# Optimization experiments

Hardware: AMD Instinct MI355X
Metric: run time of the kernel (lower is better)

The kernel has to match this reference:

```python
import jax, jax.numpy as jnp
import numpy as np

E = 1_000_000   # number of multicut edges
T = 2_000_000   # number of triplets (GNN nodes)
M = 4_000_000   # number of directed GNN edges among triplets
HID = 32


def gcn_conv(x, edge_index, W, b, n):
    """PyG GCNConv: x' = D^-1/2 (A+I) D^-1/2 (x W) + b, symmetric norm with self-loops."""
    src, dst = edge_index[0], edge_index[1]
    xw = x @ W                                        # [n, out]
    deg = jnp.zeros((n,), xw.dtype).at[dst].add(1.0) + 1.0  # +1 self-loop
    dis = jax.lax.rsqrt(deg)                          # deg^-1/2
    norm = dis[src] * dis[dst]                        # [M]
    msg = xw[src] * norm[:, None]                     # gather + scale
    out = jax.ops.segment_sum(msg, dst, num_segments=n)
    out = out + xw * (dis * dis)[:, None]             # self-loop contribution
    return out + b


def setup_inputs() -> dict:
    key = jax.random.key(0)
    ks = jax.random.split(key, 16)
    inp = {
        "edge_costs": jax.random.normal(ks[0], (E,), jnp.float32),
        "t12": jax.random.normal(ks[1], (T,), jnp.float32),
        "t13": jax.random.normal(ks[2], (T,), jnp.float32),
        "t23": jax.random.normal(ks[3], (T,), jnp.float32),
        "corr_12": jax.random.randint(ks[4], (T,), 0, E),
        "corr_13": jax.random.randint(ks[5], (T,), 0, E),
        "corr_23": jax.random.randint(ks[6], (T,), 0, E),
        # counts >= 1 so the divide is well-defined (as in real triplet decompositions)
        "edge_counter": jax.random.randint(ks[7], (E,), 1, 6).astype(jnp.float32),
        "edge_index": jax.random.randint(ks[8], (2, M), 0, T),
        # GCNConv / Linear parameters (glorot-ish scale)
        "W1": jax.random.normal(ks[9], (3, HID), jnp.float32) * (1.0 / np.sqrt(3)),
        "b1": jnp.zeros((HID,), jnp.float32),
        "W2": jax.random.normal(ks[10], (HID, HID), jnp.float32) * (1.0 / np.sqrt(HID)),
        "b2": jnp.zeros((HID,), jnp.float32),
        "Wout": jax.random.normal(ks[11], (HID, 3), jnp.float32) * (1.0 / np.sqrt(HID)),
        "bout": jnp.zeros((3,), jnp.float32),
    }
    return inp


def reference(edge_costs, t12, t13, t23, corr_12, corr_13, corr_23,
              edge_counter, edge_index, W1, b1, W2, b2, Wout, bout):
    # --- send_messages_to_triplets: gather / divide, then zero covered edges ---
    t12 = t12 + edge_costs[corr_12] / edge_counter[corr_12]
    t13 = t13 + edge_costs[corr_13] / edge_counter[corr_13]
    t23 = t23 + edge_costs[corr_23] / edge_counter[corr_23]
    edge_costs = jnp.where(edge_counter > 0, jnp.zeros_like(edge_costs), edge_costs)

    # --- send_messages_to_edges: 2-layer GCN over triplet nodes + linear head ---
    tri = jnp.stack([t12, t13, t23], axis=1)          # [T, 3]
    x = jax.nn.relu(gcn_conv(tri, edge_index, W1, b1, T))
    x = jax.nn.relu(gcn_conv(x, edge_index, W2, b2, T))
    delta = x @ Wout + bout                           # [T, 3]

    t12 = t12 - delta[:, 0]
    t13 = t13 - delta[:, 1]
    t23 = t23 - delta[:, 2]

    edge_updates = (jnp.zeros_like(edge_costs)
                    .at[corr_12].add(delta[:, 0])
                    .at[corr_13].add(delta[:, 1])
                    .at[corr_23].add(delta[:, 2]))
    edge_costs = edge_costs + edge_updates
    return (edge_costs, t12, t13, t23)
```

## Files before the change

### kernel.cpp

```cpp
#include <hip/hip_runtime.h>
#include <hip/hip_fp16.h>
#include <math.h>

#define HID 32
#define BS 256

#define NPB 4096
#define NBK_MAX 1024
#define EBT 8192
#define CAP 11776

#define NPB_E 2048

typedef _Float16 h2v __attribute__((ext_vector_type(2)));

__device__ __forceinline__ h2v u2h(uint u) { return __builtin_bit_cast(h2v, u); }
__device__ __forceinline__ uint h2u(h2v h) { return __builtin_bit_cast(uint, h); }
__device__ __forceinline__ uint pack2(float a, float b) {
  h2v r; r.x = (_Float16)a; r.y = (_Float16)b; return h2u(r);
}
__device__ __forceinline__ float dot2acc(uint a, uint b, float c) {
#if __has_builtin(__builtin_amdgcn_fdot2)
  return __builtin_amdgcn_fdot2(u2h(a), u2h(b), c, false);
#else
  h2v ah = u2h(a), bh = u2h(b);
  c = fmaf((float)ah.x, (float)bh.x, c);
  return fmaf((float)ah.y, (float)bh.y, c);
#endif
}
__device__ __forceinline__ float h4w(uint2 g) {
  h2v hi = u2h(g.y); return (float)hi.y;
}


__global__ __launch_bounds__(BS) void k_bhist2(const int* __restrict__ ei,
                                               int* __restrict__ thist, int M, int NBK) {
  __shared__ int hist[NBK_MAX];
  for (int b = threadIdx.x; b < NBK; b += BS) hist[b] = 0;
  __syncthreads();
  int e0 = blockIdx.x * EBT;
  int n = min(EBT, M - e0);
  for (int k = threadIdx.x; k < n; k += BS) {
    int d = ei[M + e0 + k];
    atomicAdd(&hist[d / NPB], 1);
  }
  __syncthreads();
  for (int b = threadIdx.x; b < NBK; b += BS)
    thist[blockIdx.x * NBK + b] = hist[b];
}

__global__ __launch_bounds__(BS) void k_ehist2(const int* __restrict__ c12,
                                               const int* __restrict__ c13,
                                               const int* __restrict__ c23,
                                               int* __restrict__ thist, int T, int NBK) {
  __shared__ int hist[NBK_MAX];
  for (int b = threadIdx.x; b < NBK; b += BS) hist[b] = 0;
  __syncthreads();
  int N3 = 3 * T;
  int j0 = blockIdx.x * EBT;
  int n = min(EBT, N3 - j0);
  for (int k = threadIdx.x; k < n; k += BS) {
    int j = j0 + k;
    int key = (j < T) ? c12[j] : ((j < 2 * T) ? c13[j - T] : c23[j - 2 * T]);
    atomicAdd(&hist[key / NPB_E], 1);
  }
  __syncthreads();
  for (int b = threadIdx.x; b < NBK; b += BS)
    thist[blockIdx.x * NBK + b] = hist[b];
}

__global__ __launch_bounds__(BS) void k_tbase(const int* __restrict__ thist,
                                              int* __restrict__ tbase,
                                              int* __restrict__ gh, int NBK, int NT) {
  __shared__ int part[BS];
  int b = blockIdx.x;
  int C = (NT + BS - 1) / BS;
  int s = 0;
  for (int k = 0; k < C; ++k) {
    int t = threadIdx.x * C + k;
    if (t < NT) s += thist[t * NBK + b];
  }
  part[threadIdx.x] = s;
  __syncthreads();
  for (int off = 1; off < BS; off <<= 1) {
    int v = part[threadIdx.x];
    int u = (threadIdx.x >= off) ? part[threadIdx.x - off] : 0;
    __syncthreads();
    part[threadIdx.x] = v + u;
    __syncthreads();
  }
  int run = (threadIdx.x > 0) ? part[threadIdx.x - 1] : 0;
  for (int k = 0; k < C; ++k) {
    int t = threadIdx.x * C + k;
    if (t < NT) {
      int v = thist[t * NBK + b];
      tbase[t * NBK + b] = run;
      run += v;
    }
  }
  if (threadIdx.x == BS - 1) gh[b] = run;
}

__global__ __launch_bounds__(BS) void k_bscan(const int* __restrict__ gh,
                                              int* __restrict__ gboff,
                                              int* __restrict__ gcur, int NBK) {
  __shared__ int part[BS];
  int C = (NBK + BS - 1) / BS;
  int s = 0;
  for (int k = 0; k < C; ++k) {
    int idx = threadIdx.x * C + k;
    if (idx < NBK) s += gh[idx];
  }
  part[threadIdx.x] = s;
  __syncthreads();
  for (int off = 1; off < BS; off <<= 1) {
    int v = part[threadIdx.x];
    int u = (threadIdx.x >= off) ? part[threadIdx.x - off] : 0;
    __syncthreads();
    part[threadIdx.x] = v + u;
    __syncthreads();
  }
  int run = (threadIdx.x > 0) ? part[threadIdx.x - 1] : 0;
  for (int k = 0; k < C; ++k) {
    int idx = threadIdx.x * C + k;
    if (idx < NBK) {
      gboff[idx] = run;
      gcur[idx] = run;
      run += gh[idx];
    }
  }
  if (threadIdx.x == BS - 1) gboff[NBK] = run;
}

__global__ __launch_bounds__(BS) void k_bplace(const int* __restrict__ ei,
                                               const int* __restrict__ gboff,
                                               const int* __restrict__ tbase,
                                               int2* __restrict__ P, int M, int NBK) {
  __shared__ int cur[NBK_MAX];
  int t = blockIdx.x;
  for (int b = threadIdx.x; b < NBK; b += BS)
    cur[b] = gboff[b] + tbase[t * NBK + b];
  __syncthreads();
  int e0 = t * EBT;
  int n = min(EBT, M - e0);
  for (int k = threadIdx.x; k < n; k += BS) {
    int sidx = ei[e0 + k];
    int d = ei[M + e0 + k];
    int pos = atomicAdd(&cur[d / NPB], 1);
    P[pos] = make_int2(sidx, d);
  }
}

__global__ __launch_bounds__(BS) void k_escatv(const int* __restrict__ c12,
                                               const int* __restrict__ c13,
                                               const int* __restrict__ c23,
                                               const float* __restrict__ dd,
                                               const int* __restrict__ gboff,
                                               const int* __restrict__ tbase,
                                               int2* __restrict__ PEV, int T, int NBK) {
  __shared__ int cur[NBK_MAX];
  int t = blockIdx.x;
  for (int b = threadIdx.x; b < NBK; b += BS)
    cur[b] = gboff[b] + tbase[t * NBK + b];
  __syncthreads();
  int N3 = 3 * T;
  int j0 = t * EBT;
  int n = min(EBT, N3 - j0);
  for (int k = threadIdx.x; k < n; k += BS) {
    int j = j0 + k;
    int key = (j < T) ? c12[j] : ((j < 2 * T) ? c13[j - T] : c23[j - 2 * T]);
    float v = dd[j];
    int pos = atomicAdd(&cur[key / NPB_E], 1);
    PEV[pos] = make_int2(key, __builtin_bit_cast(int, v));
  }
}


__global__ __launch_bounds__(BS) void k_bfinal(const int2* __restrict__ P,
                                               const int* __restrict__ gboff,
                                               int* __restrict__ row_ptr,
                                               int* __restrict__ srt, int T, int M,
                                               int NBK) {
  __shared__ int cnt[NPB];
  __shared__ int lsrt[CAP];
  __shared__ int part[BS];
  int b = blockIdx.x;
  int d0 = b * NPB;
  int nodesHere = min(NPB, T - d0);
  int p0 = gboff[b], p1 = gboff[b + 1];
  int nE = p1 - p0;
  for (int j = threadIdx.x; j < NPB; j += BS) cnt[j] = 0;
  __syncthreads();
  for (int j = threadIdx.x; j < nE; j += BS) {
    int2 p = P[p0 + j];
    atomicAdd(&cnt[p.y - d0], 1);
  }
  __syncthreads();
  const int CN = NPB / BS;
  int s = 0;
#pragma unroll
  for (int k = 0; k < CN; ++k) s += cnt[threadIdx.x * CN + k];
  part[threadIdx.x] = s;
  __syncthreads();
  for (int off = 1; off < BS; off <<= 1) {
    int v = part[threadIdx.x];
    int u = (threadIdx.x >= off) ? part[threadIdx.x - off] : 0;
    __syncthreads();
    part[threadIdx.x] = v + u;
    __syncthreads();
  }
  int run = (threadIdx.x > 0) ? part[threadIdx.x - 1] : 0;
#pragma unroll
  for (int k = 0; k < CN; ++k) {
    int idx = threadIdx.x * CN + k;
    int c = cnt[idx];
    cnt[idx] = run;
    if (idx < nodesHere) row_ptr[d0 + idx] = p0 + run;
    run += c;
  }
  if (b == NBK - 1 && threadIdx.x == 0) row_ptr[T] = M;
  __syncthreads();
  if (nE <= CAP) {
    for (int j = threadIdx.x; j < nE; j += BS) {
      int2 p = P[p0 + j];
      int pos = atomicAdd(&cnt[p.y - d0], 1);
      lsrt[pos] = p.x;
    }
    __syncthreads();
    for (int j = threadIdx.x; j < nE; j += BS) srt[p0 + j] = lsrt[j];
  } else {
    for (int j = threadIdx.x; j < nE; j += BS) {
      int2 p = P[p0 + j];
      int pos = atomicAdd(&cnt[p.y - d0], 1);
      srt[p0 + pos] = p.x;
    }
  }
}

__global__ __launch_bounds__(BS) void k_oecsum2(const int2* __restrict__ PEV,
                                                const int* __restrict__ gboff,
                                                float* __restrict__ oec, int E) {
  __shared__ float acc[NPB_E];
  int b = blockIdx.x;
  int e0 = b * NPB_E;
  int p0 = gboff[b], p1 = gboff[b + 1];
  int n = p1 - p0;
  for (int j = threadIdx.x; j < NPB_E; j += BS) acc[j] = 0.0f;
  __syncthreads();
  int k = threadIdx.x;
  for (; k + 3 * BS < n; k += 4 * BS) {
    int2 q0 = PEV[p0 + k];
    int2 q1 = PEV[p0 + k + BS];
    int2 q2 = PEV[p0 + k + 2 * BS];
    int2 q3 = PEV[p0 + k + 3 * BS];
    atomicAdd(&acc[q0.x - e0], __builtin_bit_cast(float, q0.y));
    atomicAdd(&acc[q1.x - e0], __builtin_bit_cast(float, q1.y));
    atomicAdd(&acc[q2.x - e0], __builtin_bit_cast(float, q2.y));
    atomicAdd(&acc[q3.x - e0], __builtin_bit_cast(float, q3.y));
  }
  for (; k < n; k += BS) {
    int2 q = PEV[p0 + k];
    atomicAdd(&acc[q.x - e0], __builtin_bit_cast(float, q.y));
  }
  __syncthreads();
  int lim = min(NPB_E, E - e0);
  for (int j = threadIdx.x; j < lim; j += BS) oec[e0 + j] += acc[j];
}


__global__ void k_prep_e(const float* __restrict__ ec, const float* __restrict__ cnt,
                         float* __restrict__ msg, float* __restrict__ oec, int E) {
  int i = blockIdx.x * BS + threadIdx.x;
  if (i >= E) return;
  float c = cnt[i], v = ec[i];
  msg[i] = v / c;
  oec[i] = (c > 0.0f) ? 0.0f : v;
}

__global__ void k_step1pack(const float* __restrict__ msg,
                            const float* __restrict__ t12, const float* __restrict__ t13,
                            const float* __restrict__ t23,
                            const int* __restrict__ c12, const int* __restrict__ c13,
                            const int* __restrict__ c23,
                            const int* __restrict__ row_ptr,
                            float4* __restrict__ tri4, uint2* __restrict__ trih, int T) {
  int i = blockIdx.x * BS + threadIdx.x;
  if (i >= T) return;
  int a = c12[i], b = c13[i], c = c23[i];
  float4 v;
  v.x = t12[i] + msg[a];
  v.y = t13[i] + msg[b];
  v.z = t23[i] + msg[c];
  v.w = rsqrtf((float)(row_ptr[i + 1] - row_ptr[i]) + 1.0f);
  tri4[i] = v;
  uint2 h;
  h.x = pack2(v.x, v.y);
  h.y = pack2(v.z, v.w);
  trih[i] = h;
}

__global__ void k_packw(const float* __restrict__ W1, const float* __restrict__ b1,
                        const float* __restrict__ W2, uint* __restrict__ pkw) {
  int i = blockIdx.x * BS + threadIdx.x;
  if (i < 48) {
    int r = i >> 4, k = i & 15;
    pkw[i] = pack2(W1[r * HID + 2 * k], W1[r * HID + 2 * k + 1]);
  } else if (i < 64) {
    int k = i - 48;
    pkw[i] = pack2(b1[2 * k], b1[2 * k + 1]);
  } else if (i < 576) {
    int idx = i - 64;
    int h2 = idx >> 5, j = idx & 31;
    pkw[i] = pack2(W2[(2 * h2) * HID + j], W2[(2 * h2 + 1) * HID + j]);
  }
}

__device__ __forceinline__ void acc3(uint2 g, float di, float& ax, float& ay, float& az) {
  h2v lo = u2h(g.x), hi = u2h(g.y);
  float w = (float)hi.y * di;
  ax = fmaf((float)lo.x, w, ax);
  ay = fmaf((float)lo.y, w, ay);
  az = fmaf((float)hi.x, w, az);
}

__global__ __launch_bounds__(BS) void k_agg1c(const int* __restrict__ row_ptr,
                                              const int* __restrict__ srt,
                                              const float4* __restrict__ tri4,
                                              const uint2* __restrict__ trih,
                                              uint2* __restrict__ G4h, int T) {
  int i = blockIdx.x * BS + threadIdx.x;
  if (i >= T) return;
  int r0 = row_ptr[i], r1 = row_ptr[i + 1];
  float4 ts = tri4[i];
  float di = ts.w;
  float d2 = di * di;
  float ax = ts.x * d2, ay = ts.y * d2, az = ts.z * d2;
  int e = r0;
  for (; e + 4 <= r1; e += 4) {
    int s0 = srt[e + 0];
    int s1 = srt[e + 1];
    int s2 = srt[e + 2];
    int s3 = srt[e + 3];
    uint2 g0 = trih[s0];
    uint2 g1 = trih[s1];
    uint2 g2 = trih[s2];
    uint2 g3 = trih[s3];
    acc3(g0, di, ax, ay, az);
    acc3(g1, di, ax, ay, az);
    acc3(g2, di, ax, ay, az);
    acc3(g3, di, ax, ay, az);
  }
  for (; e < r1; ++e) {
    uint2 g = trih[srt[e]];
    acc3(g, di, ax, ay, az);
  }
  uint2 o;
  o.x = pack2(ax, ay);
  o.y = pack2(az, di);
  G4h[i] = o;
}

__device__ __forceinline__ void edge_h1_accu(uint2 g, float w,
                                             const uint* __restrict__ W1s,
                                             const uint* __restrict__ b1s,
                                             float* S) {
  h2v lo = u2h(g.x), hi = u2h(g.y);
  h2v hx; hx.x = lo.x; hx.y = lo.x;
  h2v hy; hy.x = lo.y; hy.y = lo.y;
  h2v hz; hz.x = hi.x; hz.y = hi.x;
  h2v zero; zero.x = (_Float16)0.f; zero.y = (_Float16)0.f;
#pragma unroll
  for (int k = 0; k < 16; ++k) {
    h2v t = hx * u2h(W1s[k]) + (hy * u2h(W1s[16 + k]) + (hz * u2h(W1s[32 + k]) + u2h(b1s[k])));
    t = __builtin_elementwise_max(t, zero);
    S[2 * k]     = fmaf((float)t.x, w, S[2 * k]);
    S[2 * k + 1] = fmaf((float)t.y, w, S[2 * k + 1]);
  }
}

__global__ __launch_bounds__(BS) void k_l2head(
    const int* __restrict__ row_ptr, const int* __restrict__ srt,
    const uint2* __restrict__ G4h, const float4* __restrict__ tri4,
    const uint* __restrict__ pkw,
    const float* __restrict__ b2,
    const float* __restrict__ Wout, const float* __restrict__ bout,
    float* __restrict__ o12, float* __restrict__ o13, float* __restrict__ o23,
    float* __restrict__ dd, int T) {
  int i = blockIdx.x * BS + threadIdx.x;
  if (i >= T) return;
  int r0 = row_ptr[i], r1 = row_ptr[i + 1];
  uint2 gs = G4h[i];
  float4 tp = tri4[i];
  float di = tp.w;
  const uint* W1s = pkw;
  const uint* b1s = pkw + 48;
  const uint* W2s = pkw + 64;

  float S[HID];
#pragma unroll
  for (int h = 0; h < HID; ++h) S[h] = 0.0f;

  edge_h1_accu(gs, di * di, W1s, b1s, S);

  int e = r0;
  for (; e + 4 <= r1; e += 4) {
    int s0 = srt[e + 0];
    int s1 = srt[e + 1];
    int s2 = srt[e + 2];
    int s3 = srt[e + 3];
    uint2 g0 = G4h[s0];
    uint2 g1 = G4h[s1];
    uint2 g2 = G4h[s2];
    uint2 g3 = G4h[s3];
    float w0 = h4w(g0) * di;
    float w1 = h4w(g1) * di;
    float w2 = h4w(g2) * di;
    float w3 = h4w(g3) * di;
    edge_h1_accu(g0, w0, W1s, b1s, S);
    edge_h1_accu(g1, w1, W1s, b1s, S);
    edge_h1_accu(g2, w2, W1s, b1s, S);
    edge_h1_accu(g3, w3, W1s, b1s, S);
  }
  if (e + 2 <= r1) {
    int s0 = srt[e + 0];
    int s1 = srt[e + 1];
    uint2 g0 = G4h[s0];
    uint2 g1 = G4h[s1];
    float w0 = h4w(g0) * di;
    float w1 = h4w(g1) * di;
    edge_h1_accu(g0, w0, W1s, b1s, S);
    edge_h1_accu(g1, w1, W1s, b1s, S);
    e += 2;
  }
  if (e < r1) {
    uint2 g = G4h[srt[e]];
    edge_h1_accu(g, h4w(g) * di, W1s, b1s, S);
  }

  uint sh[16];
#pragma unroll
  for (int k = 0; k < 16; ++k) sh[k] = pack2(S[2 * k], S[2 * k + 1]);

  float d0 = bout[0], d1 = bout[1], dd2 = bout[2];
#pragma unroll
  for (int cz = 0; cz < 4; ++cz) {
    float z[8];
#pragma unroll
    for (int j = 0; j < 8; ++j) z[j] = b2[cz * 8 + j];
#pragma unroll
    for (int h2 = 0; h2 < 16; ++h2) {
#pragma unroll
      for (int j = 0; j < 8; ++j)
        z[j] = dot2acc(sh[h2], W2s[h2 * HID + cz * 8 + j], z[j]);
    }
#pragma unroll
    for (int j = 0; j < 8; ++j) {
      float v = fmaxf(z[j], 0.0f);
      int jp = cz * 8 + j;
      d0  = fmaf(v, Wout[jp * 3 + 0], d0);
      d1  = fmaf(v, Wout[jp * 3 + 1], d1);
      dd2 = fmaf(v, Wout[jp * 3 + 2], dd2);
    }
  }

  o12[i] = tp.x - d0;
  o13[i] = tp.y - d1;
  o23[i] = tp.z - dd2;
  dd[i] = d0;
  dd[T + i] = d1;
  dd[2 * T + i] = dd2;
}


extern "C" void kernel_launch(void* const* d_in, const int* in_sizes, int n_in,
                              void* d_out, int out_size, void* d_ws, size_t ws_size,
                              hipStream_t stream) {
  const float* ec  = (const float*)d_in[0];
  const float* t12 = (const float*)d_in[1];
  const float* t13 = (const float*)d_in[2];
  const float* t23 = (const float*)d_in[3];
  const int* c12   = (const int*)d_in[4];
  const int* c13   = (const int*)d_in[5];
  const int* c23   = (const int*)d_in[6];
  const float* cnt = (const float*)d_in[7];
  const int* ei    = (const int*)d_in[8];
  const float* W1  = (const float*)d_in[9];
  const float* b1  = (const float*)d_in[10];
  const float* W2  = (const float*)d_in[11];
  const float* b2  = (const float*)d_in[12];
  const float* Wout = (const float*)d_in[13];
  const float* bout = (const float*)d_in[14];

  const int E = in_sizes[0];
  const int T = in_sizes[1];
  const int M = in_sizes[8] / 2;
  const int NBK = (T + NPB - 1) / NPB;
  const int NBK_E = (E + NPB_E - 1) / NPB_E;

  float* oec = (float*)d_out;
  float* o12 = oec + E;
  float* o13 = o12 + T;
  float* o23 = o13 + T;

  auto blocks = [](long n) { return (int)((n + BS - 1) / BS); };
  const int tiles   = (M + EBT - 1) / EBT;
  const int tiles_e = (3 * T + EBT - 1) / EBT;

  float4* tri4 = (float4*)d_ws;
  uint2*  trih = (uint2*)(tri4 + T);
  uint2*  G4h  = trih + T;
  int2*   PEV  = (int2*)(G4h + T);
  float*  dd   = (float*)(PEV + 3 * (size_t)T);
  int*    srt  = (int*)(dd + 3 * (size_t)T);
  int*    rptr = srt + M;
  float*  msg  = (float*)(rptr + (T + 1));
  int*    gh   = (int*)(msg + E);
  int*    gboff = gh + NBK;
  int*    gcur  = gboff + (NBK + 1);
  uint*   pkw   = (uint*)(gcur + NBK);
  int*    gh_e  = (int*)(pkw + 576);
  int*    gboff_e = gh_e + NBK_E;
  int*    gcur_e  = gboff_e + (NBK_E + 1);
  int*    thist_n = gcur_e + NBK_E;
  int*    tbase_n = thist_n + (size_t)tiles * NBK;
  int*    thist_e = tbase_n + (size_t)tiles * NBK;
  int*    tbase_e = thist_e + (size_t)tiles_e * NBK_E;
  int2*   P    = (int2*)tri4;

  k_bhist2<<<tiles, BS, 0, stream>>>(ei, thist_n, M, NBK);
  k_tbase<<<NBK, BS, 0, stream>>>(thist_n, tbase_n, gh, NBK, tiles);
  k_bscan<<<1, BS, 0, stream>>>(gh, gboff, gcur, NBK);
  k_bplace<<<tiles, BS, 0, stream>>>(ei, gboff, tbase_n, P, M, NBK);
  k_bfinal<<<NBK, BS, 0, stream>>>(P, gboff, rptr, srt, T, M, NBK);

  k_ehist2<<<tiles_e, BS, 0, stream>>>(c12, c13, c23, thist_e, T, NBK_E);
  k_tbase<<<NBK_E, BS, 0, stream>>>(thist_e, tbase_e, gh_e, NBK_E, tiles_e);
  k_bscan<<<1, BS, 0, stream>>>(gh_e, gboff_e, gcur_e, NBK_E);

  k_packw<<<3, BS, 0, stream>>>(W1, b1, W2, pkw);
  k_prep_e<<<blocks(E), BS, 0, stream>>>(ec, cnt, msg, oec, E);
  k_step1pack<<<blocks(T), BS, 0, stream>>>(msg, t12, t13, t23, c12, c13, c23,
                                            rptr, tri4, trih, T);

  k_agg1c<<<blocks(T), BS, 0, stream>>>(rptr, srt, tri4, trih, G4h, T);

  k_l2head<<<blocks(T), BS, 0, stream>>>(rptr, srt, G4h, tri4, pkw,
                                         b2, Wout, bout,
                                         o12, o13, o23, dd, T);

  k_escatv<<<tiles_e, BS, 0, stream>>>(c12, c13, c23, dd, gboff_e, tbase_e,
                                       PEV, T, NBK_E);
  k_oecsum2<<<NBK_E, BS, 0, stream>>>(PEV, gboff_e, oec, E);
}
```

Baseline: 618.3 us.

## Pack bucket entries into 32-bit words and drop fp32 triplet buffer

Bucket placement now stores each GCN edge as one 32-bit word: the local destination offset sits in the high 11 bits and the 21-bit source index in the low bits. To make this fit, the bucket width is halved and the shared-memory staging capacity is reduced. The fp32 float4 triplet buffer is removed, and both aggregation kernels and the output now read the fp16-packed triplet values. This cuts memory traffic and workspace use, but the final t12/t13/t23 outputs pick up fp16 rounding error, and source indices must stay below 2^21.

```diff
diff --git a/kernel.cpp b/kernel.cpp
--- a/kernel.cpp
+++ b/kernel.cpp
@@ -5,10 +5,10 @@
 #define HID 32
 #define BS 256
 
-#define NPB 4096
+#define NPB 2048
 #define NBK_MAX 1024
 #define EBT 8192
-#define CAP 11776
+#define CAP 6912
 
 #define NPB_E 2048
 
@@ -135,7 +135,7 @@
 __global__ __launch_bounds__(BS) void k_bplace(const int* __restrict__ ei,
                                                const int* __restrict__ gboff,
                                                const int* __restrict__ tbase,
-                                               int2* __restrict__ P, int M, int NBK) {
+                                               uint* __restrict__ P, int M, int NBK) {
   __shared__ int cur[NBK_MAX];
   int t = blockIdx.x;
   for (int b = threadIdx.x; b < NBK; b += BS)
@@ -144,10 +144,10 @@
   int e0 = t * EBT;
   int n = min(EBT, M - e0);
   for (int k = threadIdx.x; k < n; k += BS) {
-    int sidx = ei[e0 + k];
+    uint sidx = (uint)ei[e0 + k];
     int d = ei[M + e0 + k];
     int pos = atomicAdd(&cur[d / NPB], 1);
-    P[pos] = make_int2(sidx, d);
+    P[pos] = ((uint)(d & (NPB - 1)) << 21) | sidx;
   }
 }
 
@@ -176,7 +176,7 @@
 }
 
 
-__global__ __launch_bounds__(BS) void k_bfinal(const int2* __restrict__ P,
+__global__ __launch_bounds__(BS) void k_bfinal(const uint* __restrict__ P,
                                                const int* __restrict__ gboff,
                                                int* __restrict__ row_ptr,
                                                int* __restrict__ srt, int T, int M,
@@ -192,8 +192,8 @@
   for (int j = threadIdx.x; j < NPB; j += BS) cnt[j] = 0;
   __syncthreads();
   for (int j = threadIdx.x; j < nE; j += BS) {
-    int2 p = P[p0 + j];
-    atomicAdd(&cnt[p.y - d0], 1);
+    uint p = P[p0 + j];
+    atomicAdd(&cnt[p >> 21], 1);
   }
   __syncthreads();
   const int CN = NPB / BS;
@@ -222,17 +222,17 @@
   __syncthreads();
   if (nE <= CAP) {
     for (int j = threadIdx.x; j < nE; j += BS) {
-      int2 p = P[p0 + j];
-      int pos = atomicAdd(&cnt[p.y - d0], 1);
-      lsrt[pos] = p.x;
+      uint p = P[p0 + j];
+      int pos = atomicAdd(&cnt[p >> 21], 1);
+      lsrt[pos] = (int)(p & 0x1FFFFFu);
     }
     __syncthreads();
     for (int j = threadIdx.x; j < nE; j += BS) srt[p0 + j] = lsrt[j];
   } else {
     for (int j = threadIdx.x; j < nE; j += BS) {
-      int2 p = P[p0 + j];
-      int pos = atomicAdd(&cnt[p.y - d0], 1);
-      srt[p0 + pos] = p.x;
+      uint p = P[p0 + j];
+      int pos = atomicAdd(&cnt[p >> 21], 1);
+      srt[p0 + pos] = (int)(p & 0x1FFFFFu);
     }
   }
 }
@@ -283,19 +283,17 @@
                             const int* __restrict__ c12, const int* __restrict__ c13,
                             const int* __restrict__ c23,
                             const int* __restrict__ row_ptr,
-                            float4* __restrict__ tri4, uint2* __restrict__ trih, int T) {
+                            uint2* __restrict__ trih, int T) {
   int i = blockIdx.x * BS + threadIdx.x;
   if (i >= T) return;
   int a = c12[i], b = c13[i], c = c23[i];
-  float4 v;
-  v.x = t12[i] + msg[a];
-  v.y = t13[i] + msg[b];
-  v.z = t23[i] + msg[c];
-  v.w = rsqrtf((float)(row_ptr[i + 1] - row_ptr[i]) + 1.0f);
-  tri4[i] = v;
+  float vx = t12[i] + msg[a];
+  float vy = t13[i] + msg[b];
+  float vz = t23[i] + msg[c];
+  float vw = rsqrtf((float)(row_ptr[i + 1] - row_ptr[i]) + 1.0f);
   uint2 h;
-  h.x = pack2(v.x, v.y);
-  h.y = pack2(v.z, v.w);
+  h.x = pack2(vx, vy);
+  h.y = pack2(vz, vw);
   trih[i] = h;
 }
 
@@ -325,16 +323,16 @@
 
 __global__ __launch_bounds__(BS) void k_agg1c(const int* __restrict__ row_ptr,
                                               const int* __restrict__ srt,
-                                              const float4* __restrict__ tri4,
                                               const uint2* __restrict__ trih,
                                               uint2* __restrict__ G4h, int T) {
   int i = blockIdx.x * BS + threadIdx.x;
   if (i >= T) return;
   int r0 = row_ptr[i], r1 = row_ptr[i + 1];
-  float4 ts = tri4[i];
-  float di = ts.w;
+  uint2 ts = trih[i];
+  h2v tlo = u2h(ts.x), thi = u2h(ts.y);
+  float di = (float)thi.y;
   float d2 = di * di;
-  float ax = ts.x * d2, ay = ts.y * d2, az = ts.z * d2;
+  float ax = (float)tlo.x * d2, ay = (float)tlo.y * d2, az = (float)thi.x * d2;
   int e = r0;
   for (; e + 4 <= r1; e += 4) {
     int s0 = srt[e + 0];
@@ -380,7 +378,7 @@
 
 __global__ __launch_bounds__(BS) void k_l2head(
     const int* __restrict__ row_ptr, const int* __restrict__ srt,
-    const uint2* __restrict__ G4h, const float4* __restrict__ tri4,
+    const uint2* __restrict__ G4h, const uint2* __restrict__ trih,
     const uint* __restrict__ pkw,
     const float* __restrict__ b2,
     const float* __restrict__ Wout, const float* __restrict__ bout,
@@ -390,8 +388,9 @@
   if (i >= T) return;
   int r0 = row_ptr[i], r1 = row_ptr[i + 1];
   uint2 gs = G4h[i];
-  float4 tp = tri4[i];
-  float di = tp.w;
+  uint2 tp = trih[i];
+  h2v tlo = u2h(tp.x), thi = u2h(tp.y);
+  float di = (float)thi.y;
   const uint* W1s = pkw;
   const uint* b1s = pkw + 48;
   const uint* W2s = pkw + 64;
@@ -463,9 +462,9 @@
     }
   }
 
-  o12[i] = tp.x - d0;
-  o13[i] = tp.y - d1;
-  o23[i] = tp.z - dd2;
+  o12[i] = (float)tlo.x - d0;
+  o13[i] = (float)tlo.y - d1;
+  o23[i] = (float)thi.x - dd2;
   dd[i] = d0;
   dd[T + i] = d1;
   dd[2 * T + i] = dd2;
@@ -506,8 +505,7 @@
   const int tiles   = (M + EBT - 1) / EBT;
   const int tiles_e = (3 * T + EBT - 1) / EBT;
 
-  float4* tri4 = (float4*)d_ws;
-  uint2*  trih = (uint2*)(tri4 + T);
+  uint2*  trih = (uint2*)d_ws;
   uint2*  G4h  = trih + T;
   int2*   PEV  = (int2*)(G4h + T);
   float*  dd   = (float*)(PEV + 3 * (size_t)T);
@@ -525,7 +523,7 @@
   int*    tbase_n = thist_n + (size_t)tiles * NBK;
   int*    thist_e = tbase_n + (size_t)tiles * NBK;
   int*    tbase_e = thist_e + (size_t)tiles_e * NBK_E;
-  int2*   P    = (int2*)tri4;
+  uint*   P    = (uint*)PEV;
 
   k_bhist2<<<tiles, BS, 0, stream>>>(ei, thist_n, M, NBK);
   k_tbase<<<NBK, BS, 0, stream>>>(thist_n, tbase_n, gh, NBK, tiles);
@@ -540,11 +538,11 @@
   k_packw<<<3, BS, 0, stream>>>(W1, b1, W2, pkw);
   k_prep_e<<<blocks(E), BS, 0, stream>>>(ec, cnt, msg, oec, E);
   k_step1pack<<<blocks(T), BS, 0, stream>>>(msg, t12, t13, t23, c12, c13, c23,
-                                            rptr, tri4, trih, T);
-
-  k_agg1c<<<blocks(T), BS, 0, stream>>>(rptr, srt, tri4, trih, G4h, T);
-
-  k_l2head<<<blocks(T), BS, 0, stream>>>(rptr, srt, G4h, tri4, pkw,
+                                            rptr, trih, T);
+
+  k_agg1c<<<blocks(T), BS, 0, stream>>>(rptr, srt, trih, G4h, T);
+
+  k_l2head<<<blocks(T), BS, 0, stream>>>(rptr, srt, G4h, trih, pkw,
                                          b2, Wout, bout,
                                          o12, o13, o23, dd, T);
 
```

After: 594.8 us. 1.04x faster.
